# Kernel optimization log

Measured on AMD Instinct MI355X. Metric: run time of the kernel, lower is better.

The kernel has to match this reference:

```python
import jax, jax.numpy as jnp
import numpy as np

RES_SCALE = 1.0

def prelu(x, a):
    return jnp.maximum(x, 0) + a * jnp.minimum(x, 0)

def conv1x1_prelu(x, w, b, a):
    # x: [N,C,H,W], w: [O,C], b: [O]
    y = jnp.einsum('nchw,oc->nohw', x, w) + b[None, :, None, None]
    return prelu(y, a)

def setup_inputs() -> dict:
    key = jax.random.key(0)
    ks = jax.random.split(key, 5)
    N, C, H, W = 2, 128, 96, 96
    Cr = C // 2  # reduction = 2
    return {
        'x':  jax.random.normal(ks[0], (N, C, H, W), jnp.float32),
        'w1': jax.random.normal(ks[1], (Cr, C), jnp.float32) * (1.0 / np.sqrt(C)),
        'b1': jnp.zeros((Cr,), jnp.float32),
        'a1': jnp.asarray(0.25, jnp.float32),
        'w2': jax.random.normal(ks[2], (Cr, C), jnp.float32) * (1.0 / np.sqrt(C)),
        'b2': jnp.zeros((Cr,), jnp.float32),
        'a2': jnp.asarray(0.25, jnp.float32),
        'wa': jax.random.normal(ks[3], (C, C), jnp.float32) * (1.0 / np.sqrt(C)),
        'ba': jnp.zeros((C,), jnp.float32),
        'aa': jnp.asarray(0.25, jnp.float32),
    }

def reference(x, w1, b1, a1, w2, b2, a2, wa, ba, aa):
    N, C, H, W = x.shape
    q = conv1x1_prelu(x, w1, b1, a1)   # [N,Cr,H,W]
    k = conv1x1_prelu(x, w2, b2, a2)   # [N,Cr,H,W]
    v = conv1x1_prelu(x, wa, ba, aa)   # [N,C,H,W]
    Cr = q.shape[1]
    L = H * W
    q = q.transpose(0, 2, 3, 1).reshape(N, L, Cr)   # [N,L,Cr]
    k = k.reshape(N, Cr, L)                          # [N,Cr,L]
    score = jax.nn.softmax(jnp.matmul(q, k), axis=2)  # [N,L,L]
    v = v.reshape(N, C, L).transpose(0, 2, 1)        # [N,L,C]
    out = jnp.matmul(score, v)                        # [N,L,C]
    out = out.transpose(0, 2, 1).reshape(N, C, H, W)
    return out + RES_SCALE * x
```

## Files before the change

kernel.cpp:

```cpp
#include <hip/hip_runtime.h>

#define N_  2
#define C_  128
#define CR_ 64
#define H_  96
#define W_  96
#define L_  (H_*W_)
#define QBLK 128
#define KVBLK 64
#define NQB (L_/QBLK)
#define SPLITS 8
#define TILES_PER ((L_/KVBLK)/SPLITS)
#define NCHUNK (N_*NQB*SPLITS)
#define LOG2E 1.44269504088896f

typedef short bf16x8 __attribute__((ext_vector_type(8)));
typedef float f32x4  __attribute__((ext_vector_type(4)));

static __device__ __forceinline__ float exp2_fast(float x) {
    return __builtin_amdgcn_exp2f(x);
}

static __device__ __forceinline__ unsigned short f2bf(float f) {
    unsigned u = __builtin_bit_cast(unsigned, f);
    unsigned rounding = 0x7FFFu + ((u >> 16) & 1u);
    return (unsigned short)((u + rounding) >> 16);
}

static __device__ __forceinline__ unsigned cvt_pk_bf16(float lo, float hi) {
    unsigned r;
    asm("v_cvt_pk_bf16_f32 %0, %1, %2" : "=v"(r) : "v"(lo), "v"(hi));
    return r;
}

static __device__ __forceinline__ float bf2f(unsigned short s) {
    return __builtin_bit_cast(float, ((unsigned)s) << 16);
}

static __device__ __forceinline__ int sigma_(int r) {
    return (r & 0x23) | ((r & 0x0C) << 1) | ((r & 0x10) >> 2);
}

#define GLD16(G, Ld) __builtin_amdgcn_global_load_lds( \
    (const __attribute__((address_space(1))) void*)(G), \
    (__attribute__((address_space(3))) void*)(Ld), 16, 0, 0)

__global__ __launch_bounds__(256) void wconv_kernel(
    const float* __restrict__ w1, const float* __restrict__ b1, const float* __restrict__ a1,
    const float* __restrict__ w2, const float* __restrict__ b2, const float* __restrict__ a2,
    const float* __restrict__ wa, const float* __restrict__ ba, const float* __restrict__ aa,
    unsigned short* __restrict__ Wbf,
    float* __restrict__ bias, float* __restrict__ alpha, float* __restrict__ scale)
{
    const int idx = blockIdx.x * 256 + threadIdx.x;
    const int o = idx >> 7, k = idx & 127;
    float wv;
    if (o < 64)       wv = w1[o*C_ + k];
    else if (o < 128) wv = w2[(o-64)*C_ + k];
    else              wv = wa[(o-128)*C_ + k];
    Wbf[idx] = f2bf(wv);
    if (blockIdx.x == 0) {
        int t = threadIdx.x;
        float b, a, sc;
        if (t < 64)       { b = b1[t];       a = a1[0]; sc = LOG2E; }
        else if (t < 128) { b = b2[t-64];    a = a2[0]; sc = 1.0f; }
        else              { b = ba[t-128];   a = aa[0]; sc = 1.0f; }
        bias[t] = b; alpha[t] = a; scale[t] = sc;
    }
}

__global__ __launch_bounds__(256) void proj_mfma_kernel(
    const float* __restrict__ x,
    const unsigned short* __restrict__ Wbf,
    const float* __restrict__ bias,
    const float* __restrict__ alpha,
    const float* __restrict__ scale,
    unsigned short* __restrict__ qkv)
{
    __shared__ alignas(16) unsigned char xs[64 * 256];

    const int blk  = blockIdx.x;
    const int n    = blk / (L_/64);
    const int i0   = (blk % (L_/64)) * 64;
    const float* xb = x + (size_t)n * C_ * L_;
    const int tid  = threadIdx.x;
    const int wv_  = tid >> 6;
    const int lane = tid & 63;
    const int lhi  = lane >> 4;
    const int llo  = lane & 15;

    {
        const int i = lane;
        #pragma unroll
        for (int p = 0; p < 8; p++) {
            int c0 = wv_*4 + p*16;
            float v0 = xb[(size_t)(c0+0)*L_ + i0 + i];
            float v1 = xb[(size_t)(c0+1)*L_ + i0 + i];
            float v2 = xb[(size_t)(c0+2)*L_ + i0 + i];
            float v3 = xb[(size_t)(c0+3)*L_ + i0 + i];
            uint2 pk2;
            pk2.x = cvt_pk_bf16(v0, v1);
            pk2.y = cvt_pk_bf16(v2, v3);
            int byte = i*256 + ((((c0 >> 3) ^ (i & 7))) << 4) + (c0 & 7) * 2;
            *reinterpret_cast<uint2*>(xs + byte) = pk2;
        }
    }
    __syncthreads();

    bf16x8 xf[4][4];
    #pragma unroll
    for (int it = 0; it < 4; it++) {
        int i = it*16 + llo;
        #pragma unroll
        for (int ks = 0; ks < 4; ks++) {
            int byte = i*256 + (((ks*4 + lhi) ^ (i & 7)) << 4);
            xf[it][ks] = *reinterpret_cast<const bf16x8*>(xs + byte);
        }
    }

    unsigned short* q_t = qkv;
    unsigned short* k_t = qkv + (size_t)N_ * L_ * CR_;
    unsigned short* v   = qkv + (size_t)2 * N_ * L_ * CR_;
    unsigned short* qtb = q_t + (size_t)n * L_ * CR_;
    unsigned short* ktb = k_t + (size_t)n * L_ * CR_;
    unsigned short* vb  = v   + (size_t)n * C_ * L_;

    #pragma unroll
    for (int oo = 0; oo < 2; oo++) {
        const int ot = wv_*2 + oo;
        const unsigned short* wrow = Wbf + (size_t)(ot*16 + llo) * 128;
        bf16x8 wf[4];
        #pragma unroll
        for (int ks = 0; ks < 4; ks++)
            wf[ks] = *reinterpret_cast<const bf16x8*>(wrow + ks*32 + lhi*8);
        f32x4 acc[4];
        #pragma unroll
        for (int it = 0; it < 4; it++) acc[it] = f32x4{0.f, 0.f, 0.f, 0.f};
        #pragma unroll
        for (int ks = 0; ks < 4; ks++)
            #pragma unroll
            for (int it = 0; it < 4; it++)
                acc[it] = __builtin_amdgcn_mfma_f32_16x16x32_bf16(wf[ks], xf[it][ks], acc[it], 0, 0, 0);

        const int ob = ot*16 + lhi*4;
        const float4 b4 = *reinterpret_cast<const float4*>(bias  + ob);
        const float4 a4 = *reinterpret_cast<const float4*>(alpha + ob);
        const float4 s4 = *reinterpret_cast<const float4*>(scale + ob);
        unsigned short* dst = (ot < 4) ? qtb : ktb;
        const int col = (ot & 3)*16 + lhi*4;
        #pragma unroll
        for (int it = 0; it < 4; it++) {
            int i = i0 + it*16 + llo;
            float y0 = acc[it][0] + b4.x; y0 = (fmaxf(y0,0.f) + a4.x*fminf(y0,0.f))*s4.x;
            float y1 = acc[it][1] + b4.y; y1 = (fmaxf(y1,0.f) + a4.y*fminf(y1,0.f))*s4.y;
            float y2 = acc[it][2] + b4.z; y2 = (fmaxf(y2,0.f) + a4.z*fminf(y2,0.f))*s4.z;
            float y3 = acc[it][3] + b4.w; y3 = (fmaxf(y3,0.f) + a4.w*fminf(y3,0.f))*s4.w;
            uint2 pk2;
            pk2.x = cvt_pk_bf16(y0, y1);
            pk2.y = cvt_pk_bf16(y2, y3);
            *reinterpret_cast<uint2*>(dst + (size_t)i * CR_ + col) = pk2;
        }
    }

    #pragma unroll
    for (int oo = 0; oo < 2; oo++) {
        const int ot2 = wv_*2 + oo;
        const int op  = ot2*16 + llo;
        const unsigned short* wrow = Wbf + (size_t)(128 + op) * 128;
        bf16x8 wf[4];
        #pragma unroll
        for (int ks = 0; ks < 4; ks++)
            wf[ks] = *reinterpret_cast<const bf16x8*>(wrow + ks*32 + lhi*8);
        f32x4 acc[4];
        #pragma unroll
        for (int it = 0; it < 4; it++) acc[it] = f32x4{0.f, 0.f, 0.f, 0.f};
        #pragma unroll
        for (int ks = 0; ks < 4; ks++)
            #pragma unroll
            for (int it = 0; it < 4; it++)
                acc[it] = __builtin_amdgcn_mfma_f32_16x16x32_bf16(xf[it][ks], wf[ks], acc[it], 0, 0, 0);

        const float b = bias[128 + op];
        const float a = alpha[128 + op];
        #pragma unroll
        for (int it = 0; it < 4; it++) {
            float y0 = acc[it][0] + b; y0 = fmaxf(y0,0.f) + a*fminf(y0,0.f);
            float y1 = acc[it][1] + b; y1 = fmaxf(y1,0.f) + a*fminf(y1,0.f);
            float y2 = acc[it][2] + b; y2 = fmaxf(y2,0.f) + a*fminf(y2,0.f);
            float y3 = acc[it][3] + b; y3 = fmaxf(y3,0.f) + a*fminf(y3,0.f);
            uint2 pk2;
            pk2.x = cvt_pk_bf16(y0, y1);
            pk2.y = cvt_pk_bf16(y2, y3);
            *reinterpret_cast<uint2*>(vb + (size_t)op * L_ + i0 + it*16 + lhi*4) = pk2;
        }
    }
}

__global__ __launch_bounds__(256, 3) void attn_kernel(
    const unsigned short* __restrict__ qkv,
    unsigned short* __restrict__ o_part,
    float* __restrict__ l_part)
{
    __shared__ alignas(16) unsigned char kv_lds[2][24*1024];

    const unsigned short* q_t = qkv;
    const unsigned short* k_t = qkv + (size_t)N_ * L_ * CR_;
    const unsigned short* v   = qkv + (size_t)2 * N_ * L_ * CR_;

    const int blk  = blockIdx.x;
    const int n    = blk / (NQB * SPLITS);
    const int rem  = blk % (NQB * SPLITS);
    const int qbi  = rem / SPLITS;
    const int s    = rem % SPLITS;
    const int qb   = qbi * QBLK;
    const int tid  = threadIdx.x;
    const int wave = tid >> 6;
    const int lane = tid & 63;
    const int lhi  = lane >> 4;
    const int llo  = lane & 15;

    const int jb_beg = s * TILES_PER * KVBLK;
    const int jb_end = jb_beg + TILES_PER * KVBLK;

    const unsigned short* qtb = q_t + (size_t)n * L_ * CR_;
    const unsigned short* ktb = k_t + (size_t)n * L_ * CR_;
    const unsigned short* vb  = v   + (size_t)n * C_ * L_;

    bf16x8 qf[2][2];
    #pragma unroll
    for (int st = 0; st < 2; st++) {
        int row = qb + wave * 32 + st * 16 + llo;
        #pragma unroll
        for (int ks = 0; ks < 2; ks++)
            qf[st][ks] = *reinterpret_cast<const bf16x8*>(qtb + (size_t)row * CR_ + ks*32 + lhi*8);
    }

    bf16x8 ones_f;
    #pragma unroll
    for (int e = 0; e < 8; e++) ones_f[e] = (short)0x3F80;

    const int l8 = lane >> 3;
    const int l7 = (lane & 7) * 16;
    const int rho0 = wave*16 + l8;
    const int rho1 = rho0 + 8;
    const unsigned short* kbase0 = ktb + (size_t)sigma_(rho0) * CR_ + ((l7 ^ ((rho0 & 7) << 4)) >> 1);
    const unsigned short* kbase1 = ktb + (size_t)sigma_(rho1) * CR_ + ((l7 ^ ((rho1 & 7) << 4)) >> 1);
    const unsigned short* vbase[4];
    #pragma unroll
    for (int vt = 0; vt < 4; vt++) {
        int c = wave*32 + vt*8 + l8;
        vbase[vt] = vb + (size_t)c * L_ + ((l7 ^ (l8 << 4)) >> 1);
    }

    #define STAGE(b, jb_) do {                                                   \
        GLD16(kbase0 + (size_t)(jb_) * CR_, &kv_lds[b][(wave*2+0)*1024 + 0]);    \
        GLD16(kbase1 + (size_t)(jb_) * CR_, &kv_lds[b][(wave*2+1)*1024 + 0]);    \
        GLD16(vbase[0] + (jb_), &kv_lds[b][8192 + (wave*4+0)*1024]);             \
        GLD16(vbase[1] + (jb_), &kv_lds[b][8192 + (wave*4+1)*1024]);             \
        GLD16(vbase[2] + (jb_), &kv_lds[b][8192 + (wave*4+2)*1024]);             \
        GLD16(vbase[3] + (jb_), &kv_lds[b][8192 + (wave*4+3)*1024]);             \
    } while (0)

    f32x4 o_acc[2][8];
    #pragma unroll
    for (int st = 0; st < 2; st++)
        #pragma unroll
        for (int ct = 0; ct < 8; ct++) o_acc[st][ct] = f32x4{0.f, 0.f, 0.f, 0.f};
    f32x4 acc_l[2];
    acc_l[0] = f32x4{0.f, 0.f, 0.f, 0.f};
    acc_l[1] = f32x4{0.f, 0.f, 0.f, 0.f};

    int cur = 0;
    STAGE(0, jb_beg);
    __syncthreads();

    for (int jb = jb_beg; jb < jb_end; jb += KVBLK) {
        if (jb + KVBLK < jb_end) STAGE(cur ^ 1, jb + KVBLK);

        const unsigned char* kbuf = &kv_lds[cur][0];
        const unsigned char* vbuf = &kv_lds[cur][8192];

        f32x4 sacc[2][4];
        #pragma unroll
        for (int st = 0; st < 2; st++)
            #pragma unroll
            for (int jt = 0; jt < 4; jt++) sacc[st][jt] = f32x4{0.f, 0.f, 0.f, 0.f};
        __builtin_amdgcn_s_setprio(1);
        #pragma unroll
        for (int ks = 0; ks < 2; ks++) {
            #pragma unroll
            for (int jt = 0; jt < 4; jt++) {
                int rho  = jt*16 + llo;
                int colb = ks*64 + lhi*16;
                bf16x8 kf = *reinterpret_cast<const bf16x8*>(
                    kbuf + rho*128 + (colb ^ ((rho & 7) << 4)));
                sacc[0][jt] = __builtin_amdgcn_mfma_f32_16x16x32_bf16(kf, qf[0][ks], sacc[0][jt], 0, 0, 0);
                sacc[1][jt] = __builtin_amdgcn_mfma_f32_16x16x32_bf16(kf, qf[1][ks], sacc[1][jt], 0, 0, 0);
            }
        }
        __builtin_amdgcn_s_setprio(0);

        #pragma unroll
        for (int st = 0; st < 2; st++)
            #pragma unroll
            for (int jt = 0; jt < 4; jt++)
                #pragma unroll
                for (int r = 0; r < 4; r++)
                    sacc[st][jt][r] = exp2_fast(sacc[st][jt][r]);

        __builtin_amdgcn_s_setprio(1);
        #pragma unroll
        for (int ks = 0; ks < 2; ks++) {
            unsigned pw0[4], pw1[4];
            pw0[0] = cvt_pk_bf16(sacc[0][2*ks][0],   sacc[0][2*ks][1]);
            pw0[1] = cvt_pk_bf16(sacc[0][2*ks][2],   sacc[0][2*ks][3]);
            pw0[2] = cvt_pk_bf16(sacc[0][2*ks+1][0], sacc[0][2*ks+1][1]);
            pw0[3] = cvt_pk_bf16(sacc[0][2*ks+1][2], sacc[0][2*ks+1][3]);
            pw1[0] = cvt_pk_bf16(sacc[1][2*ks][0],   sacc[1][2*ks][1]);
            pw1[1] = cvt_pk_bf16(sacc[1][2*ks][2],   sacc[1][2*ks][3]);
            pw1[2] = cvt_pk_bf16(sacc[1][2*ks+1][0], sacc[1][2*ks+1][1]);
            pw1[3] = cvt_pk_bf16(sacc[1][2*ks+1][2], sacc[1][2*ks+1][3]);
            bf16x8 pf0 = *reinterpret_cast<const bf16x8*>(&pw0[0]);
            bf16x8 pf1 = *reinterpret_cast<const bf16x8*>(&pw1[0]);
            acc_l[0] = __builtin_amdgcn_mfma_f32_16x16x32_bf16(ones_f, pf0, acc_l[0], 0, 0, 0);
            acc_l[1] = __builtin_amdgcn_mfma_f32_16x16x32_bf16(ones_f, pf1, acc_l[1], 0, 0, 0);
            #pragma unroll
            for (int ct = 0; ct < 8; ct++) {
                int c = ct*16 + llo;
                int colb = ks*64 + lhi*16;
                bf16x8 vf = *reinterpret_cast<const bf16x8*>(
                    vbuf + c*128 + (colb ^ ((c & 7) << 4)));
                o_acc[0][ct] = __builtin_amdgcn_mfma_f32_16x16x32_bf16(vf, pf0, o_acc[0][ct], 0, 0, 0);
                o_acc[1][ct] = __builtin_amdgcn_mfma_f32_16x16x32_bf16(vf, pf1, o_acc[1][ct], 0, 0, 0);
            }
        }
        __builtin_amdgcn_s_setprio(0);

        __syncthreads();
        cur ^= 1;
    }
    #undef STAGE

    unsigned short* ob = o_part + (size_t)blk * (QBLK*C_);
    float* lb = l_part + (size_t)blk * QBLK;
    #pragma unroll
    for (int st = 0; st < 2; st++) {
        int i_loc = wave*32 + st*16 + llo;
        #pragma unroll
        for (int ct = 0; ct < 8; ct++) {
            uint2 pkd;
            pkd.x = cvt_pk_bf16(o_acc[st][ct][0], o_acc[st][ct][1]);
            pkd.y = cvt_pk_bf16(o_acc[st][ct][2], o_acc[st][ct][3]);
            *reinterpret_cast<uint2*>(ob + ((size_t)ct * QBLK + i_loc) * 16 + lhi*4) = pkd;
        }
        if (lhi == 0) lb[i_loc] = acc_l[st][0];
    }
}

__global__ __launch_bounds__(256) void combine_kernel(
    const unsigned short* __restrict__ o_part,
    const float* __restrict__ l_part,
    const float* __restrict__ x,
    float* __restrict__ out)
{
    __shared__ float invl[32];

    const int blk  = blockIdx.x;
    const int part = blk & 3;
    const int qbi  = (blk >> 2) % NQB;
    const int n    = blk / (4 * NQB);
    const int tid  = threadIdx.x;
    const int i0   = part * 32;

    const size_t pbase = (size_t)(n*NQB + qbi) * SPLITS;

    if (tid < 32) {
        float lt = 0.f;
        for (int s = 0; s < SPLITS; s++)
            lt += l_part[(pbase + s) * QBLK + i0 + tid];
        invl[tid] = 1.0f / lt;
    }
    __syncthreads();

    const int il = tid & 31;
    const int cg = tid >> 5;

    float acc[16];
    #pragma unroll
    for (int k = 0; k < 16; k++) acc[k] = 0.f;

    for (int s = 0; s < SPLITS; s++) {
        const unsigned short* src = o_part + (pbase + s) * (QBLK*C_)
                                  + ((size_t)cg * QBLK + i0 + il) * 16;
        bf16x8 v0 = *reinterpret_cast<const bf16x8*>(src);
        bf16x8 v1 = *reinterpret_cast<const bf16x8*>(src + 8);
        #pragma unroll
        for (int k = 0; k < 8; k++) acc[k]     += bf2f((unsigned short)v0[k]);
        #pragma unroll
        for (int k = 0; k < 8; k++) acc[8 + k] += bf2f((unsigned short)v1[k]);
    }

    const float nv = invl[il];
    const int ig = qbi*QBLK + i0 + il;
    const float* xb = x   + (size_t)n * C_ * L_;
    float*       ob = out + (size_t)n * C_ * L_;
    #pragma unroll
    for (int k = 0; k < 16; k++) {
        int c = cg*16 + k;
        ob[(size_t)c * L_ + ig] = acc[k] * nv + xb[(size_t)c * L_ + ig];
    }
}

extern "C" void kernel_launch(void* const* d_in, const int* in_sizes, int n_in,
                              void* d_out, int out_size, void* d_ws, size_t ws_size,
                              hipStream_t stream) {
    const float* x  = (const float*)d_in[0];
    const float* w1 = (const float*)d_in[1];
    const float* b1 = (const float*)d_in[2];
    const float* a1 = (const float*)d_in[3];
    const float* w2 = (const float*)d_in[4];
    const float* b2 = (const float*)d_in[5];
    const float* a2 = (const float*)d_in[6];
    const float* wa = (const float*)d_in[7];
    const float* ba = (const float*)d_in[8];
    const float* aa = (const float*)d_in[9];
    float* out = (float*)d_out;

    unsigned short* qkv = (unsigned short*)d_ws;
    size_t qkv_bytes = ((size_t)2*N_*L_*CR_ + (size_t)N_*C_*L_) * 2;
    size_t off = (qkv_bytes + 255) & ~(size_t)255;

    unsigned short* o_part = (unsigned short*)((char*)d_ws + off);
    size_t o_elems = (size_t)NCHUNK * QBLK * C_;
    float* l_part = (float*)(o_part + o_elems);
    float* tail   = l_part + (size_t)NCHUNK * QBLK;
    unsigned short* Wbf = (unsigned short*)tail;
    float* bias  = (float*)(Wbf + 256*128);
    float* alpha = bias + 256;
    float* scale = alpha + 256;

    wconv_kernel<<<128, 256, 0, stream>>>(w1, b1, a1, w2, b2, a2, wa, ba, aa,
                                          Wbf, bias, alpha, scale);
    proj_mfma_kernel<<<N_ * (L_/64), 256, 0, stream>>>(x, Wbf, bias, alpha, scale, qkv);
    attn_kernel<<<NCHUNK, 256, 0, stream>>>(qkv, o_part, l_part);
    combine_kernel<<<N_ * NQB * 4, 256, 0, stream>>>(o_part, l_part, x, out);
}
```

Measured before the change: 93.88 us.

## Stage KV in 32-key halves with four-deep LDS ring and vmcnt waits

```diff
diff --git a/kernel.cpp b/kernel.cpp
--- a/kernel.cpp
+++ b/kernel.cpp
@@ -11,7 +11,9 @@
 #define NQB (L_/QBLK)
 #define SPLITS 8
 #define TILES_PER ((L_/KVBLK)/SPLITS)
+#define HALVES (TILES_PER*2)
 #define NCHUNK (N_*NQB*SPLITS)
+#define BUFSZ 12288
 #define LOG2E 1.44269504088896f
 
 typedef short bf16x8 __attribute__((ext_vector_type(8)));
@@ -37,8 +39,8 @@
     return __builtin_bit_cast(float, ((unsigned)s) << 16);
 }
 
-static __device__ __forceinline__ int sigma_(int r) {
-    return (r & 0x23) | ((r & 0x0C) << 1) | ((r & 0x10) >> 2);
+static __device__ __forceinline__ int sigma32_(int r) {
+    return ((r & 0x0C) << 1) | ((r & 0x10) >> 2) | (r & 3);
 }
 
 #define GLD16(G, Ld) __builtin_amdgcn_global_load_lds( \
@@ -201,7 +203,7 @@
     unsigned short* __restrict__ o_part,
     float* __restrict__ l_part)
 {
-    __shared__ alignas(16) unsigned char kv_lds[2][24*1024];
+    __shared__ alignas(16) unsigned char kv_lds[4*BUFSZ];
 
     const unsigned short* q_t = qkv;
     const unsigned short* k_t = qkv + (size_t)N_ * L_ * CR_;
@@ -220,7 +222,6 @@
     const int llo  = lane & 15;
 
     const int jb_beg = s * TILES_PER * KVBLK;
-    const int jb_end = jb_beg + TILES_PER * KVBLK;
 
     const unsigned short* qtb = q_t + (size_t)n * L_ * CR_;
     const unsigned short* ktb = k_t + (size_t)n * L_ * CR_;
@@ -239,27 +240,36 @@
     #pragma unroll
     for (int e = 0; e < 8; e++) ones_f[e] = (short)0x3F80;
 
-    const int l8 = lane >> 3;
-    const int l7 = (lane & 7) * 16;
-    const int rho0 = wave*16 + l8;
-    const int rho1 = rho0 + 8;
-    const unsigned short* kbase0 = ktb + (size_t)sigma_(rho0) * CR_ + ((l7 ^ ((rho0 & 7) << 4)) >> 1);
-    const unsigned short* kbase1 = ktb + (size_t)sigma_(rho1) * CR_ + ((l7 ^ ((rho1 & 7) << 4)) >> 1);
-    const unsigned short* vbase[4];
-    #pragma unroll
-    for (int vt = 0; vt < 4; vt++) {
-        int c = wave*32 + vt*8 + l8;
-        vbase[vt] = vb + (size_t)c * L_ + ((l7 ^ (l8 << 4)) >> 1);
-    }
-
-    #define STAGE(b, jb_) do {                                                   \
-        GLD16(kbase0 + (size_t)(jb_) * CR_, &kv_lds[b][(wave*2+0)*1024 + 0]);    \
-        GLD16(kbase1 + (size_t)(jb_) * CR_, &kv_lds[b][(wave*2+1)*1024 + 0]);    \
-        GLD16(vbase[0] + (jb_), &kv_lds[b][8192 + (wave*4+0)*1024]);             \
-        GLD16(vbase[1] + (jb_), &kv_lds[b][8192 + (wave*4+1)*1024]);             \
-        GLD16(vbase[2] + (jb_), &kv_lds[b][8192 + (wave*4+2)*1024]);             \
-        GLD16(vbase[3] + (jb_), &kv_lds[b][8192 + (wave*4+3)*1024]);             \
+    const unsigned short* ksrc;
+    {
+        int rho = tid >> 3, gb = tid & 7;
+        ksrc = ktb + (size_t)sigma32_(rho) * CR_ + (gb ^ (rho & 7)) * 8;
+    }
+    const unsigned short* vsrc[2];
+    #pragma unroll
+    for (int q = 0; q < 2; q++) {
+        int vi = q*256 + tid;
+        int row = vi >> 3, gb = vi & 7;
+        int glin = gb ^ (row & 7);
+        int c  = row*2 + (glin >> 2);
+        int j8 = (glin & 3) * 8;
+        vsrc[q] = vb + (size_t)c * L_ + j8;
+    }
+
+    #define ISSUE(h_) do {                                                        \
+        unsigned char* buf_ = &kv_lds[((h_) & 3) * BUFSZ];                        \
+        int j0_ = jb_beg + (h_) * 32;                                             \
+        GLD16(ksrc + (size_t)j0_ * CR_, buf_ + wave*1024);                        \
+        GLD16(vsrc[0] + j0_, buf_ + 4096 + wave*1024);                            \
+        GLD16(vsrc[1] + j0_, buf_ + 8192 + wave*1024);                            \
     } while (0)
+
+    #define WAITBAR(NN) do {                                                      \
+        asm volatile("s_waitcnt vmcnt(" #NN ")" ::: "memory");                    \
+        asm volatile("s_barrier" ::: "memory");                                   \
+    } while (0)
+
+    #define ENDBAR() asm volatile("s_barrier" ::: "memory")
 
     f32x4 o_acc[2][8];
     #pragma unroll
@@ -270,76 +280,71 @@
     acc_l[0] = f32x4{0.f, 0.f, 0.f, 0.f};
     acc_l[1] = f32x4{0.f, 0.f, 0.f, 0.f};
 
-    int cur = 0;
-    STAGE(0, jb_beg);
-    __syncthreads();
-
-    for (int jb = jb_beg; jb < jb_end; jb += KVBLK) {
-        if (jb + KVBLK < jb_end) STAGE(cur ^ 1, jb + KVBLK);
-
-        const unsigned char* kbuf = &kv_lds[cur][0];
-        const unsigned char* vbuf = &kv_lds[cur][8192];
-
-        f32x4 sacc[2][4];
-        #pragma unroll
-        for (int st = 0; st < 2; st++)
-            #pragma unroll
-            for (int jt = 0; jt < 4; jt++) sacc[st][jt] = f32x4{0.f, 0.f, 0.f, 0.f};
-        __builtin_amdgcn_s_setprio(1);
-        #pragma unroll
-        for (int ks = 0; ks < 2; ks++) {
-            #pragma unroll
-            for (int jt = 0; jt < 4; jt++) {
-                int rho  = jt*16 + llo;
-                int colb = ks*64 + lhi*16;
-                bf16x8 kf = *reinterpret_cast<const bf16x8*>(
-                    kbuf + rho*128 + (colb ^ ((rho & 7) << 4)));
-                sacc[0][jt] = __builtin_amdgcn_mfma_f32_16x16x32_bf16(kf, qf[0][ks], sacc[0][jt], 0, 0, 0);
-                sacc[1][jt] = __builtin_amdgcn_mfma_f32_16x16x32_bf16(kf, qf[1][ks], sacc[1][jt], 0, 0, 0);
-            }
-        }
-        __builtin_amdgcn_s_setprio(0);
-
-        #pragma unroll
-        for (int st = 0; st < 2; st++)
-            #pragma unroll
-            for (int jt = 0; jt < 4; jt++)
-                #pragma unroll
-                for (int r = 0; r < 4; r++)
-                    sacc[st][jt][r] = exp2_fast(sacc[st][jt][r]);
-
-        __builtin_amdgcn_s_setprio(1);
-        #pragma unroll
-        for (int ks = 0; ks < 2; ks++) {
-            unsigned pw0[4], pw1[4];
-            pw0[0] = cvt_pk_bf16(sacc[0][2*ks][0],   sacc[0][2*ks][1]);
-            pw0[1] = cvt_pk_bf16(sacc[0][2*ks][2],   sacc[0][2*ks][3]);
-            pw0[2] = cvt_pk_bf16(sacc[0][2*ks+1][0], sacc[0][2*ks+1][1]);
-            pw0[3] = cvt_pk_bf16(sacc[0][2*ks+1][2], sacc[0][2*ks+1][3]);
-            pw1[0] = cvt_pk_bf16(sacc[1][2*ks][0],   sacc[1][2*ks][1]);
-            pw1[1] = cvt_pk_bf16(sacc[1][2*ks][2],   sacc[1][2*ks][3]);
-            pw1[2] = cvt_pk_bf16(sacc[1][2*ks+1][0], sacc[1][2*ks+1][1]);
-            pw1[3] = cvt_pk_bf16(sacc[1][2*ks+1][2], sacc[1][2*ks+1][3]);
-            bf16x8 pf0 = *reinterpret_cast<const bf16x8*>(&pw0[0]);
-            bf16x8 pf1 = *reinterpret_cast<const bf16x8*>(&pw1[0]);
-            acc_l[0] = __builtin_amdgcn_mfma_f32_16x16x32_bf16(ones_f, pf0, acc_l[0], 0, 0, 0);
-            acc_l[1] = __builtin_amdgcn_mfma_f32_16x16x32_bf16(ones_f, pf1, acc_l[1], 0, 0, 0);
-            #pragma unroll
-            for (int ct = 0; ct < 8; ct++) {
-                int c = ct*16 + llo;
-                int colb = ks*64 + lhi*16;
-                bf16x8 vf = *reinterpret_cast<const bf16x8*>(
-                    vbuf + c*128 + (colb ^ ((c & 7) << 4)));
-                o_acc[0][ct] = __builtin_amdgcn_mfma_f32_16x16x32_bf16(vf, pf0, o_acc[0][ct], 0, 0, 0);
-                o_acc[1][ct] = __builtin_amdgcn_mfma_f32_16x16x32_bf16(vf, pf1, o_acc[1][ct], 0, 0, 0);
-            }
-        }
-        __builtin_amdgcn_s_setprio(0);
-
-        __syncthreads();
-        cur ^= 1;
-    }
-    #undef STAGE
+    const int kg0 = ((0*4 + lhi) ^ (llo & 7)) * 16;
+    const int kg1 = ((1*4 + lhi) ^ (llo & 7)) * 16;
+    const int vgb = (((llo & 1) * 4 + lhi) ^ ((llo >> 1) & 7)) * 16;
+    const int vrow_b = (llo >> 1) * 128;
+
+    #define COMPUTE(h_) do {                                                      \
+        const unsigned char* buf_ = &kv_lds[((h_) & 3) * BUFSZ];                  \
+        const unsigned char* kbuf_ = buf_;                                        \
+        const unsigned char* vbuf_ = buf_ + 4096;                                 \
+        f32x4 sacc[2][2];                                                         \
+        sacc[0][0] = f32x4{0.f,0.f,0.f,0.f}; sacc[0][1] = f32x4{0.f,0.f,0.f,0.f}; \
+        sacc[1][0] = f32x4{0.f,0.f,0.f,0.f}; sacc[1][1] = f32x4{0.f,0.f,0.f,0.f}; \
+        __builtin_amdgcn_s_setprio(1);                                            \
+        _Pragma("unroll")                                                         \
+        for (int ks = 0; ks < 2; ks++) {                                          \
+            const int kgb = ks ? kg1 : kg0;                                       \
+            _Pragma("unroll")                                                     \
+            for (int jt = 0; jt < 2; jt++) {                                      \
+                bf16x8 kf = *reinterpret_cast<const bf16x8*>(                     \
+                    kbuf_ + jt*2048 + llo*128 + kgb);                             \
+                sacc[0][jt] = __builtin_amdgcn_mfma_f32_16x16x32_bf16(kf, qf[0][ks], sacc[0][jt], 0, 0, 0); \
+                sacc[1][jt] = __builtin_amdgcn_mfma_f32_16x16x32_bf16(kf, qf[1][ks], sacc[1][jt], 0, 0, 0); \
+            }                                                                     \
+        }                                                                         \
+        __builtin_amdgcn_s_setprio(0);                                            \
+        unsigned pw0[4], pw1[4];                                                  \
+        pw0[0] = cvt_pk_bf16(exp2_fast(sacc[0][0][0]), exp2_fast(sacc[0][0][1])); \
+        pw0[1] = cvt_pk_bf16(exp2_fast(sacc[0][0][2]), exp2_fast(sacc[0][0][3])); \
+        pw0[2] = cvt_pk_bf16(exp2_fast(sacc[0][1][0]), exp2_fast(sacc[0][1][1])); \
+        pw0[3] = cvt_pk_bf16(exp2_fast(sacc[0][1][2]), exp2_fast(sacc[0][1][3])); \
+        pw1[0] = cvt_pk_bf16(exp2_fast(sacc[1][0][0]), exp2_fast(sacc[1][0][1])); \
+        pw1[1] = cvt_pk_bf16(exp2_fast(sacc[1][0][2]), exp2_fast(sacc[1][0][3])); \
+        pw1[2] = cvt_pk_bf16(exp2_fast(sacc[1][1][0]), exp2_fast(sacc[1][1][1])); \
+        pw1[3] = cvt_pk_bf16(exp2_fast(sacc[1][1][2]), exp2_fast(sacc[1][1][3])); \
+        bf16x8 pf0 = *reinterpret_cast<const bf16x8*>(&pw0[0]);                   \
+        bf16x8 pf1 = *reinterpret_cast<const bf16x8*>(&pw1[0]);                   \
+        __builtin_amdgcn_s_setprio(1);                                            \
+        acc_l[0] = __builtin_amdgcn_mfma_f32_16x16x32_bf16(ones_f, pf0, acc_l[0], 0, 0, 0); \
+        acc_l[1] = __builtin_amdgcn_mfma_f32_16x16x32_bf16(ones_f, pf1, acc_l[1], 0, 0, 0); \
+        _Pragma("unroll")                                                         \
+        for (int ct = 0; ct < 8; ct++) {                                          \
+            bf16x8 vf = *reinterpret_cast<const bf16x8*>(                         \
+                vbuf_ + ct*1024 + vrow_b + vgb);                                  \
+            o_acc[0][ct] = __builtin_amdgcn_mfma_f32_16x16x32_bf16(vf, pf0, o_acc[0][ct], 0, 0, 0); \
+            o_acc[1][ct] = __builtin_amdgcn_mfma_f32_16x16x32_bf16(vf, pf1, o_acc[1][ct], 0, 0, 0); \
+        }                                                                         \
+        __builtin_amdgcn_s_setprio(0);                                            \
+    } while (0)
+
+    ISSUE(0); ISSUE(1); ISSUE(2);
+
+    for (int h = 0; h < HALVES - 3; h++) {
+        ISSUE(h + 3);
+        WAITBAR(9);
+        COMPUTE(h);
+        ENDBAR();
+    }
+    WAITBAR(6); COMPUTE(HALVES - 3); ENDBAR();
+    WAITBAR(3); COMPUTE(HALVES - 2); ENDBAR();
+    WAITBAR(0); COMPUTE(HALVES - 1);
+
+    #undef ISSUE
+    #undef WAITBAR
+    #undef ENDBAR
+    #undef COMPUTE
 
     unsigned short* ob = o_part + (size_t)blk * (QBLK*C_);
     float* lb = l_part + (size_t)blk * QBLK;
```

Result: slower. 96.07 us (+2.3%).
